# Kernel tuning notes

Hardware: AMD Instinct MI355X
Metric: run time of the kernel (lower is better)

## Reference

```python
import jax, jax.numpy as jnp
import numpy as np

INPUT_DIM = 2
COUNT_BINS = 16
BOUND = 5.0
FLOW_LENGTH = 4
HIDDEN = 256
MULT = 4 * COUNT_BINS - 1  # 63 param groups per dim (w:K, h:K, d:K-1, lam:K)
MIN_BIN = 1e-3
MIN_DERIV = 1e-3
MIN_LAMBDA = 0.025
N = 131072


def _masks():
    input_idx = np.arange(1, INPUT_DIM + 1)                  # [2]
    hidden_idx = np.arange(HIDDEN) % (INPUT_DIM - 1) + 1     # all ones for input_dim=2
    out_idx = np.tile(input_idx, MULT)                       # [126] -> [1,2,1,2,...]
    m1 = (hidden_idx[:, None] >= input_idx[None, :]).astype(np.float32)   # [H,2]
    m2 = (hidden_idx[:, None] >= hidden_idx[None, :]).astype(np.float32)  # [H,H]
    m3 = (out_idx[:, None] > hidden_idx[None, :]).astype(np.float32)      # [126,H]
    return jnp.asarray(m1), jnp.asarray(m2), jnp.asarray(m3)


def _made(z, W1, b1, W2, b2, W3, b3, m1, m2, m3):
    # masked MLP producing raw spline params, shape [..., MULT, input_dim]
    h = jax.nn.relu(z @ (W1 * m1).T + b1)
    h = jax.nn.relu(h @ (W2 * m2).T + b2)
    out = (h @ (W3 * m3).T + b3).reshape(z.shape[:-1] + (MULT, INPUT_DIM))
    K = COUNT_BINS
    sw = lambda t: jnp.swapaxes(t, -1, -2)  # -> [..., input_dim, K]
    w = sw(out[..., 0:K, :])
    hh = sw(out[..., K:2 * K, :])
    d = sw(out[..., 2 * K:3 * K - 1, :])
    lam = sw(out[..., 3 * K - 1:4 * K - 1, :])
    return w, hh, d, lam


def _spline(x, w_raw, h_raw, d_raw, l_raw):
    # Pyro monotonic linear rational spline (Dolatabadi et al.), forward only.
    K = COUNT_BINS
    left, right = -BOUND, BOUND
    w = jax.nn.softmax(w_raw, axis=-1)
    h = jax.nn.softmax(h_raw, axis=-1)
    d = jax.nn.softplus(d_raw)
    l = jax.nn.sigmoid(l_raw)

    widths = MIN_BIN + (1.0 - MIN_BIN * K) * w
    zpad = jnp.zeros(widths.shape[:-1] + (1,), widths.dtype)
    cw = jnp.concatenate([zpad, jnp.cumsum(widths, -1)], -1)
    cw = (right - left) * cw + left
    cw = cw.at[..., 0].set(left).at[..., -1].set(right)
    widths = cw[..., 1:] - cw[..., :-1]

    heights = MIN_BIN + (1.0 - MIN_BIN * K) * h
    ch = jnp.concatenate([zpad, jnp.cumsum(heights, -1)], -1)
    ch = (right - left) * ch + left
    ch = ch.at[..., 0].set(left).at[..., -1].set(right)
    heights = ch[..., 1:] - ch[..., :-1]

    deriv = MIN_DERIV + d
    onep = jnp.ones(deriv.shape[:-1] + (1,), deriv.dtype)
    deriv = jnp.concatenate([onep, deriv, onep], -1)  # boundary derivs = 1, [.., K+1]

    lam = MIN_LAMBDA + (1.0 - 2.0 * MIN_LAMBDA) * l

    inside = (x >= left) & (x <= right)
    xc = jnp.clip(x, left, right)

    bin_idx = jnp.clip(jnp.sum((xc[..., None] >= cw).astype(jnp.int32), -1) - 1, 0, K - 1)
    ib = bin_idx[..., None]
    g = lambda t: jnp.take_along_axis(t, ib, -1)[..., 0]
    x_k = g(cw)
    w_k = g(widths)
    y_k = g(ch)
    h_k = g(heights)
    d_k = g(deriv)
    d_k1 = jnp.take_along_axis(deriv, ib + 1, -1)[..., 0]
    lam_k = g(lam)

    wa = 1.0
    wb = jnp.sqrt(d_k / d_k1) * wa
    wc = (lam_k * wa * d_k + (1.0 - lam_k) * wb * d_k1) * (w_k / h_k)
    ya = y_k
    yb = h_k + y_k
    yc = ((1.0 - lam_k) * wa * ya + lam_k * wb * yb) / ((1.0 - lam_k) * wa + lam_k * wb)

    theta = (xc - x_k) / w_k
    left_seg = theta <= lam_k
    num = jnp.where(left_seg,
                    wa * ya * (lam_k - theta) + wc * yc * theta,
                    wc * yc * (1.0 - theta) + wb * yb * (theta - lam_k))
    den = jnp.where(left_seg,
                    wa * (lam_k - theta) + wc * theta,
                    wc * (1.0 - theta) + wb * (theta - lam_k))
    y = num / den
    return jnp.where(inside, y, x)  # identity outside [-B, B]


def setup_inputs() -> dict:
    key = jax.random.key(0)
    ks = jax.random.split(key, 7)
    s = 0.05
    return {
        "x": jax.random.normal(ks[0], (N, INPUT_DIM), jnp.float32),
        "W1": jax.random.normal(ks[1], (HIDDEN, INPUT_DIM), jnp.float32) * s,
        "b1": jax.random.normal(ks[2], (HIDDEN,), jnp.float32) * s,
        "W2": jax.random.normal(ks[3], (HIDDEN, HIDDEN), jnp.float32) * s,
        "b2": jax.random.normal(ks[4], (HIDDEN,), jnp.float32) * s,
        "W3": jax.random.normal(ks[5], (MULT * INPUT_DIM, HIDDEN), jnp.float32) * s,
        "b3": jax.random.normal(ks[6], (MULT * INPUT_DIM,), jnp.float32) * s,
    }


def reference(x, W1, b1, W2, b2, W3, b3):
    # forward(): apply the SAME shared spline transform flow_length times,
    # collecting intermediates zs (returned stacked: [L+1, N, 2]).
    m1, m2, m3 = _masks()
    z = x
    zs = [z]
    for _ in range(FLOW_LENGTH):
        w, hh, d, l = _made(z, W1, b1, W2, b2, W3, b3, m1, m2, m3)
        z = _spline(z, w, hh, d, l)
        zs.append(z)
    return jnp.stack(zs)
```

## Files before the change

kernel.cpp:

```cpp
#include <hip/hip_runtime.h>
#include <hip/hip_fp16.h>
#include <math.h>

#define N_SAMPLES 131072
#define HIDDEN    256
#define M_GRID    2048
#define REC       144
#define U_LO      (-8.0f)
#define DELTA     0.0078125f
#define INV_DELTA 128.0f
#define MT3       16

__device__ __attribute__((aligned(16))) float g_H2T[M_GRID * HIDDEN];
__device__ __attribute__((aligned(16))) float g_table[M_GRID * REC];
__device__ __attribute__((aligned(16))) float g_knots0[REC];

__device__ __forceinline__ float rcpf(float x) { return __builtin_amdgcn_rcpf(x); }

__device__ __forceinline__ float softplusf(float x) {
  return fmaxf(x, 0.0f) + log1pf(expf(-fabsf(x)));
}

__device__ __forceinline__ void unpack8(uint4 u, float* f) {
  float2 t;
  t = __half22float2(*(__half2*)&u.x); f[0] = t.x; f[1] = t.y;
  t = __half22float2(*(__half2*)&u.y); f[2] = t.x; f[3] = t.y;
  t = __half22float2(*(__half2*)&u.z); f[4] = t.x; f[5] = t.y;
  t = __half22float2(*(__half2*)&u.w); f[6] = t.x; f[7] = t.y;
}

__device__ void process_column(const float* __restrict__ raw, int stride,
                               float* __restrict__ rec) {
  float v[16];
  float cw[17], ch[17], dv[17], lm[16];
  float mx = -1e30f;
#pragma unroll
  for (int k = 0; k < 16; k++) { v[k] = raw[k * stride]; mx = fmaxf(mx, v[k]); }
  float s = 0.0f;
#pragma unroll
  for (int k = 0; k < 16; k++) { v[k] = expf(v[k] - mx); s += v[k]; }
  float scl = 0.984f / s;
  cw[0] = -5.0f;
  float a = 0.0f;
#pragma unroll
  for (int k = 0; k < 16; k++) {
    a += fmaf(v[k], scl, 0.001f);
    cw[k + 1] = fmaf(a, 10.0f, -5.0f);
  }
  cw[16] = 5.0f;
  mx = -1e30f;
#pragma unroll
  for (int k = 0; k < 16; k++) { v[k] = raw[(16 + k) * stride]; mx = fmaxf(mx, v[k]); }
  s = 0.0f;
#pragma unroll
  for (int k = 0; k < 16; k++) { v[k] = expf(v[k] - mx); s += v[k]; }
  scl = 0.984f / s;
  ch[0] = -5.0f;
  a = 0.0f;
#pragma unroll
  for (int k = 0; k < 16; k++) {
    a += fmaf(v[k], scl, 0.001f);
    ch[k + 1] = fmaf(a, 10.0f, -5.0f);
  }
  ch[16] = 5.0f;
  dv[0] = 1.0f; dv[16] = 1.0f;
#pragma unroll
  for (int j = 0; j < 15; j++) dv[j + 1] = 0.001f + softplusf(raw[(32 + j) * stride]);
#pragma unroll
  for (int k = 0; k < 16; k++) {
    float xx = raw[(47 + k) * stride];
    lm[k] = fmaf(0.95f, 1.0f / (1.0f + expf(-xx)), 0.025f);
  }
  unsigned int kn[8];
#pragma unroll
  for (int q = 0; q < 8; q++) {
    __half2 h2 = __floats2half2_rn(cw[2 * q], cw[2 * q + 1]);
    kn[q] = *(unsigned int*)&h2;
  }
  uint4* u4 = (uint4*)rec;
  u4[0] = make_uint4(kn[0], kn[1], kn[2], kn[3]);
  u4[1] = make_uint4(kn[4], kn[5], kn[6], kn[7]);
  float4* r4 = (float4*)rec;
  r4[2] = make_float4(0.0f, 0.0f, 0.0f, 0.0f);
  r4[3] = make_float4(0.0f, 0.0f, 0.0f, 0.0f);
#pragma unroll
  for (int k = 0; k < 16; k++) {
    r4[4 + 2 * k]     = make_float4(ch[k], ch[k + 1], dv[k], dv[k + 1]);
    r4[4 + 2 * k + 1] = make_float4(lm[k], cw[k], cw[k + 1], 0.0f);
  }
}

__device__ __forceinline__ float spline_eval(float z, float xk, float xk1,
                                             float yk, float yk1,
                                             float dk, float dk1, float lam) {
  float xc = fminf(fmaxf(z, -5.0f), 5.0f);
  float wk = xk1 - xk;
  float hk = yk1 - yk;
  float wb = __builtin_amdgcn_sqrtf(dk * rcpf(dk1));
  float wc = fmaf(lam, dk, (1.0f - lam) * wb * dk1) * wk * rcpf(hk);
  float ya = yk;
  float yb = yk + hk;
  float yc = fmaf(lam * wb, yb, (1.0f - lam) * ya) * rcpf(fmaf(lam, wb, 1.0f - lam));
  float th = (xc - xk) * rcpf(wk);
  bool left = th <= lam;
  float num = left ? fmaf(ya, lam - th, wc * yc * th)
                   : fmaf(wc * yc, 1.0f - th, wb * yb * (th - lam));
  float den = left ? fmaf(wc, th, lam - th)
                   : fmaf(wc, 1.0f - th, wb * (th - lam));
  float y = num * rcpf(den);
  bool inside = (z >= -5.0f) && (z <= 5.0f);
  return inside ? y : z;
}

__global__ __launch_bounds__(256) void k_gemm2(const float* __restrict__ W1,
                                               const float* __restrict__ b1,
                                               const float* __restrict__ W2,
                                               const float* __restrict__ b2) {
  __shared__ float sW[256 * 67];
  __shared__ float2 sAB[256];
  __shared__ float red[3 * 64 * 36];
  const int t = threadIdx.x;
  const int m0 = blockIdx.x * 32;
  const int o0 = blockIdx.y * 64;
  {
    const int ol = t >> 2, seg = t & 3;
    const float* src = W2 + (size_t)(o0 + ol) * 256 + 16 * seg;
#pragma unroll
    for (int c = 0; c < 4; c++) {
#pragma unroll
      for (int q = 0; q < 4; q++) {
        float4 v = *(const float4*)(src + 64 * c + 4 * q);
        const int k = 64 * c + 16 * seg + 4 * q;
        sW[(k + 0) * 67 + ol] = v.x;
        sW[(k + 1) * 67 + ol] = v.y;
        sW[(k + 2) * 67 + ol] = v.z;
        sW[(k + 3) * 67 + ol] = v.w;
      }
    }
  }
  sAB[t] = make_float2(W1[2 * t], b1[t]);
  __syncthreads();
  const int w = t >> 6, lane = t & 63;
  const int tp = lane >> 2, tm = lane & 3;
  const float u0 = fmaf((float)(m0 + 8 * tm), DELTA, U_LO);
  float acc[4][8] = {};
  const int kb = w * 64;
#pragma unroll 8
  for (int kk = 0; kk < 64; kk++) {
    const int k = kb + kk;
    float4 av = *(const float4*)&sW[k * 67 + 4 * tp];
    float2 ab = sAB[k];
    float t0 = fmaf(ab.x, u0, ab.y);
    float st = ab.x * DELTA;
    float h[8];
#pragma unroll
    for (int j = 0; j < 8; j++) h[j] = fmaxf(fmaf((float)j, st, t0), 0.0f);
#pragma unroll
    for (int i = 0; i < 4; i++) {
      const float aa = (i == 0) ? av.x : (i == 1) ? av.y : (i == 2) ? av.z : av.w;
#pragma unroll
      for (int j = 0; j < 8; j++) acc[i][j] = fmaf(aa, h[j], acc[i][j]);
    }
  }
  if (w > 0) {
#pragma unroll
    for (int i = 0; i < 4; i++) {
      *(float4*)&red[((w - 1) * 64 + lane) * 36 + 8 * i] =
          make_float4(acc[i][0], acc[i][1], acc[i][2], acc[i][3]);
      *(float4*)&red[((w - 1) * 64 + lane) * 36 + 8 * i + 4] =
          make_float4(acc[i][4], acc[i][5], acc[i][6], acc[i][7]);
    }
  }
  __syncthreads();
  if (w == 0) {
#pragma unroll
    for (int v = 0; v < 3; v++) {
#pragma unroll
      for (int i = 0; i < 4; i++) {
        float4 r0 = *(const float4*)&red[(v * 64 + lane) * 36 + 8 * i];
        float4 r1 = *(const float4*)&red[(v * 64 + lane) * 36 + 8 * i + 4];
        acc[i][0] += r0.x; acc[i][1] += r0.y; acc[i][2] += r0.z; acc[i][3] += r0.w;
        acc[i][4] += r1.x; acc[i][5] += r1.y; acc[i][6] += r1.z; acc[i][7] += r1.w;
      }
    }
    float4 bb = *(const float4*)&b2[o0 + 4 * tp];
#pragma unroll
    for (int j = 0; j < 8; j++) {
      float4 r;
      r.x = fmaxf(acc[0][j] + bb.x, 0.0f);
      r.y = fmaxf(acc[1][j] + bb.y, 0.0f);
      r.z = fmaxf(acc[2][j] + bb.z, 0.0f);
      r.w = fmaxf(acc[3][j] + bb.w, 0.0f);
      *(float4*)&g_H2T[(size_t)(m0 + 8 * tm + j) * 256 + o0 + 4 * tp] = r;
    }
  }
}

__global__ __launch_bounds__(256) void k_gemm3proc(const float* __restrict__ W3,
                                                   const float* __restrict__ b3) {
  __shared__ float sW[256 * 67];
  __shared__ float sH[256 * 20];
  __shared__ float raws[64 * 20];
  const int t = threadIdx.x;
  const int m0 = blockIdx.x * MT3;
  {
    const int ol = t >> 2, seg = t & 3;
    const int row = (ol < 63) ? (2 * ol + 1) : 1;
    const float* src = W3 + (size_t)row * 256 + 16 * seg;
#pragma unroll
    for (int c = 0; c < 4; c++) {
#pragma unroll
      for (int q = 0; q < 4; q++) {
        float4 v = *(const float4*)(src + 64 * c + 4 * q);
        const int k = 64 * c + 16 * seg + 4 * q;
        sW[(k + 0) * 67 + ol] = v.x;
        sW[(k + 1) * 67 + ol] = v.y;
        sW[(k + 2) * 67 + ol] = v.z;
        sW[(k + 3) * 67 + ol] = v.w;
      }
    }
  }
  {
    const int j = t & 15, c = t >> 4;
    const float* src = g_H2T + (size_t)(m0 + j) * 256 + 16 * c;
#pragma unroll
    for (int q = 0; q < 4; q++) {
      float4 v = *(const float4*)(src + 4 * q);
      const int k = 16 * c + 4 * q;
      sH[(k + 0) * 20 + j] = v.x;
      sH[(k + 1) * 20 + j] = v.y;
      sH[(k + 2) * 20 + j] = v.z;
      sH[(k + 3) * 20 + j] = v.w;
    }
  }
  __syncthreads();
  const int w = t >> 6, lane = t & 63;
  const int tp = lane >> 2, tm = lane & 3;
  float acc[4][4] = {};
  const int kb = w * 64;
#pragma unroll 8
  for (int kk = 0; kk < 64; kk++) {
    const int k = kb + kk;
    float4 av = *(const float4*)&sW[k * 67 + 4 * tp];
    float4 bv = *(const float4*)&sH[k * 20 + 4 * tm];
    acc[0][0] = fmaf(av.x, bv.x, acc[0][0]); acc[0][1] = fmaf(av.x, bv.y, acc[0][1]);
    acc[0][2] = fmaf(av.x, bv.z, acc[0][2]); acc[0][3] = fmaf(av.x, bv.w, acc[0][3]);
    acc[1][0] = fmaf(av.y, bv.x, acc[1][0]); acc[1][1] = fmaf(av.y, bv.y, acc[1][1]);
    acc[1][2] = fmaf(av.y, bv.z, acc[1][2]); acc[1][3] = fmaf(av.y, bv.w, acc[1][3]);
    acc[2][0] = fmaf(av.z, bv.x, acc[2][0]); acc[2][1] = fmaf(av.z, bv.y, acc[2][1]);
    acc[2][2] = fmaf(av.z, bv.z, acc[2][2]); acc[2][3] = fmaf(av.z, bv.w, acc[2][3]);
    acc[3][0] = fmaf(av.w, bv.x, acc[3][0]); acc[3][1] = fmaf(av.w, bv.y, acc[3][1]);
    acc[3][2] = fmaf(av.w, bv.z, acc[3][2]); acc[3][3] = fmaf(av.w, bv.w, acc[3][3]);
  }
  __syncthreads();
  if (w > 0) {
#pragma unroll
    for (int i = 0; i < 4; i++)
      *(float4*)&sH[((w - 1) * 64 + lane) * 20 + 4 * i] =
          make_float4(acc[i][0], acc[i][1], acc[i][2], acc[i][3]);
  }
  __syncthreads();
  if (w == 0) {
#pragma unroll
    for (int v = 0; v < 3; v++) {
#pragma unroll
      for (int i = 0; i < 4; i++) {
        float4 r = *(const float4*)&sH[(v * 64 + lane) * 20 + 4 * i];
        acc[i][0] += r.x; acc[i][1] += r.y; acc[i][2] += r.z; acc[i][3] += r.w;
      }
    }
#pragma unroll
    for (int i = 0; i < 4; i++) {
      const int p = 4 * tp + i;
      const int bi = (p < 63) ? (2 * p + 1) : 1;
      const float bias = b3[bi];
      *(float4*)&raws[p * 20 + 4 * tm] =
          make_float4(acc[i][0] + bias, acc[i][1] + bias,
                      acc[i][2] + bias, acc[i][3] + bias);
    }
  }
  __syncthreads();
  if (t < MT3) process_column(&raws[t], 20, g_table + (size_t)(m0 + t) * REC);
  if (t == 64 && blockIdx.x == 0) process_column(b3, 2, g_knots0);
}

__global__ __launch_bounds__(256) void k_main(const float* __restrict__ x,
                                              float* __restrict__ out) {
  __shared__ __attribute__((aligned(16))) float kn0[REC];
  for (int j = threadIdx.x; j < REC; j += 256) kn0[j] = g_knots0[j];
  __syncthreads();
  float kf0[16];
  {
    uint4 q0 = *(const uint4*)(kn0);
    uint4 q1 = *(const uint4*)(kn0 + 4);
    unpack8(q0, kf0);
    unpack8(q1, kf0 + 8);
  }
  const int i = blockIdx.x * 256 + threadIdx.x;
  const float2 xv = ((const float2*)x)[i];
  float z0 = xv.x, z1 = xv.y;
  ((float2*)out)[i] = xv;
  for (int t = 0; t < 4; t++) {
    float tt = (z0 - U_LO) * INV_DELTA;
    int i0 = (int)floorf(tt);
    i0 = min(max(i0, 0), M_GRID - 2);
    float f = fminf(fmaxf(tt - (float)i0, 0.0f), 1.0f);
    const float* r0 = g_table + (size_t)i0 * REC;
    float kf[16];
    {
      uint4 q0 = *(const uint4*)(r0);
      uint4 q1 = *(const uint4*)(r0 + 4);
      unpack8(q0, kf);
      unpack8(q1, kf + 8);
    }
    float xc1 = fminf(fmaxf(z1, -5.0f), 5.0f);
    int k1 = 0;
#pragma unroll
    for (int j = 1; j < 16; j++) k1 += (xc1 >= kf[j]) ? 1 : 0;
    const float* c0 = r0 + 16 + 8 * k1;
    float4 A0 = *(const float4*)c0;
    float4 A1 = *(const float4*)(c0 + 4);
    float4 B0 = *(const float4*)(c0 + REC);
    float4 B1 = *(const float4*)(c0 + REC + 4);
    float yk  = fmaf(f, B0.x - A0.x, A0.x);
    float yk1 = fmaf(f, B0.y - A0.y, A0.y);
    float dk  = fmaf(f, B0.z - A0.z, A0.z);
    float dk1 = fmaf(f, B0.w - A0.w, A0.w);
    float lam = fmaf(f, B1.x - A1.x, A1.x);
    float xk  = fmaf(f, B1.y - A1.y, A1.y);
    float xk1 = fmaf(f, B1.z - A1.z, A1.z);
    float z1n = spline_eval(z1, xk, xk1, yk, yk1, dk, dk1, lam);
    float xc0 = fminf(fmaxf(z0, -5.0f), 5.0f);
    int k0 = 0;
#pragma unroll
    for (int j = 1; j < 16; j++) k0 += (xc0 >= kf0[j]) ? 1 : 0;
    const float* c = kn0 + 16 + 8 * k0;
    float4 C0 = *(const float4*)c;
    float4 C1 = *(const float4*)(c + 4);
    float z0n = spline_eval(z0, C1.y, C1.z, C0.x, C0.y, C0.z, C0.w, C1.x);
    z0 = z0n; z1 = z1n;
    ((float2*)(out + (size_t)(t + 1) * (N_SAMPLES * 2)))[i] = make_float2(z0, z1);
  }
}

extern "C" void kernel_launch(void* const* d_in, const int* in_sizes, int n_in,
                              void* d_out, int out_size, void* d_ws, size_t ws_size,
                              hipStream_t stream) {
  const float* x  = (const float*)d_in[0];
  const float* W1 = (const float*)d_in[1];
  const float* b1 = (const float*)d_in[2];
  const float* W2 = (const float*)d_in[3];
  const float* b2 = (const float*)d_in[4];
  const float* W3 = (const float*)d_in[5];
  const float* b3 = (const float*)d_in[6];
  float* out = (float*)d_out;
  hipLaunchKernelGGL(k_gemm2, dim3(M_GRID / 32, 4), dim3(256), 0, stream, W1, b1, W2, b2);
  hipLaunchKernelGGL(k_gemm3proc, dim3(M_GRID / MT3), dim3(256), 0, stream, W3, b3);
  hipLaunchKernelGGL(k_main, dim3(N_SAMPLES / 256), dim3(256), 0, stream, x, out);
}
```

Baseline: 104.1 us.

## Store weights, hidden activations and spline table in packed fp16

Packs W2/W3 and the hidden activations into half2 in shared memory for both GEMM kernels, halving LDS footprint and read traffic per k-step. The spline lookup table records are also stored as half2, shrinking REC from 144 to 72 floats so the sampler's gathers fetch one uint4 per row instead of two float4s. This lowers shared-memory use and global table bandwidth, but adds conversion instructions and brings fp16 rounding error into the GEMM inputs and spline parameters, including knot positions and y-values.

Result: no change. 103.1 us (-1.0%).

```diff
diff --git a/kernel.cpp b/kernel.cpp
--- a/kernel.cpp
+++ b/kernel.cpp
@@ -5,11 +5,12 @@
 #define N_SAMPLES 131072
 #define HIDDEN    256
 #define M_GRID    2048
-#define REC       144
+#define REC       72
 #define U_LO      (-8.0f)
 #define DELTA     0.0078125f
 #define INV_DELTA 128.0f
 #define MT3       16
+#define STR2      69
 
 __device__ __attribute__((aligned(16))) float g_H2T[M_GRID * HIDDEN];
 __device__ __attribute__((aligned(16))) float g_table[M_GRID * REC];
@@ -19,6 +20,11 @@
 
 __device__ __forceinline__ float softplusf(float x) {
   return fmaxf(x, 0.0f) + log1pf(expf(-fabsf(x)));
+}
+
+__device__ __forceinline__ unsigned int packh2(float a, float b) {
+  __half2 h = __floats2half2_rn(a, b);
+  return *(unsigned int*)&h;
 }
 
 __device__ __forceinline__ void unpack8(uint4 u, float* f) {
@@ -71,22 +77,15 @@
     float xx = raw[(47 + k) * stride];
     lm[k] = fmaf(0.95f, 1.0f / (1.0f + expf(-xx)), 0.025f);
   }
-  unsigned int kn[8];
-#pragma unroll
-  for (int q = 0; q < 8; q++) {
-    __half2 h2 = __floats2half2_rn(cw[2 * q], cw[2 * q + 1]);
-    kn[q] = *(unsigned int*)&h2;
-  }
   uint4* u4 = (uint4*)rec;
-  u4[0] = make_uint4(kn[0], kn[1], kn[2], kn[3]);
-  u4[1] = make_uint4(kn[4], kn[5], kn[6], kn[7]);
-  float4* r4 = (float4*)rec;
-  r4[2] = make_float4(0.0f, 0.0f, 0.0f, 0.0f);
-  r4[3] = make_float4(0.0f, 0.0f, 0.0f, 0.0f);
+  u4[0] = make_uint4(packh2(cw[0], cw[1]),  packh2(cw[2], cw[3]),
+                     packh2(cw[4], cw[5]),  packh2(cw[6], cw[7]));
+  u4[1] = make_uint4(packh2(cw[8], cw[9]),  packh2(cw[10], cw[11]),
+                     packh2(cw[12], cw[13]), packh2(cw[14], cw[15]));
 #pragma unroll
   for (int k = 0; k < 16; k++) {
-    r4[4 + 2 * k]     = make_float4(ch[k], ch[k + 1], dv[k], dv[k + 1]);
-    r4[4 + 2 * k + 1] = make_float4(lm[k], cw[k], cw[k + 1], 0.0f);
+    u4[2 + k] = make_uint4(packh2(ch[k], ch[k + 1]), packh2(dv[k], dv[k + 1]),
+                           packh2(lm[k], cw[k]),     packh2(cw[k + 1], 0.0f));
   }
 }
 
@@ -116,7 +115,7 @@
                                                const float* __restrict__ b1,
                                                const float* __restrict__ W2,
                                                const float* __restrict__ b2) {
-  __shared__ float sW[256 * 67];
+  __shared__ unsigned int sW[128 * STR2];
   __shared__ float2 sAB[256];
   __shared__ float red[3 * 64 * 36];
   const int t = threadIdx.x;
@@ -130,11 +129,9 @@
 #pragma unroll
       for (int q = 0; q < 4; q++) {
         float4 v = *(const float4*)(src + 64 * c + 4 * q);
-        const int k = 64 * c + 16 * seg + 4 * q;
-        sW[(k + 0) * 67 + ol] = v.x;
-        sW[(k + 1) * 67 + ol] = v.y;
-        sW[(k + 2) * 67 + ol] = v.z;
-        sW[(k + 3) * 67 + ol] = v.w;
+        const int k2 = (64 * c + 16 * seg + 4 * q) >> 1;
+        sW[(k2 + 0) * STR2 + ol] = packh2(v.x, v.y);
+        sW[(k2 + 1) * STR2 + ol] = packh2(v.z, v.w);
       }
     }
   }
@@ -144,22 +141,35 @@
   const int tp = lane >> 2, tm = lane & 3;
   const float u0 = fmaf((float)(m0 + 8 * tm), DELTA, U_LO);
   float acc[4][8] = {};
-  const int kb = w * 64;
-#pragma unroll 8
-  for (int kk = 0; kk < 64; kk++) {
-    const int k = kb + kk;
-    float4 av = *(const float4*)&sW[k * 67 + 4 * tp];
-    float2 ab = sAB[k];
-    float t0 = fmaf(ab.x, u0, ab.y);
-    float st = ab.x * DELTA;
-    float h[8];
-#pragma unroll
-    for (int j = 0; j < 8; j++) h[j] = fmaxf(fmaf((float)j, st, t0), 0.0f);
-#pragma unroll
-    for (int i = 0; i < 4; i++) {
-      const float aa = (i == 0) ? av.x : (i == 1) ? av.y : (i == 2) ? av.z : av.w;
-#pragma unroll
-      for (int j = 0; j < 8; j++) acc[i][j] = fmaf(aa, h[j], acc[i][j]);
+  const int kb2 = w * 32;
+#pragma unroll 4
+  for (int kk = 0; kk < 32; kk++) {
+    const int k2 = kb2 + kk;
+    uint4 ap = *(const uint4*)&sW[k2 * STR2 + 4 * tp];
+    float2 a0 = __half22float2(*(__half2*)&ap.x);
+    float2 a1 = __half22float2(*(__half2*)&ap.y);
+    float2 a2 = __half22float2(*(__half2*)&ap.z);
+    float2 a3 = __half22float2(*(__half2*)&ap.w);
+    float2 abe = sAB[2 * k2];
+    float2 abo = sAB[2 * k2 + 1];
+    float t0e = fmaf(abe.x, u0, abe.y), ste = abe.x * DELTA;
+    float t0o = fmaf(abo.x, u0, abo.y), sto = abo.x * DELTA;
+    float he[8], ho[8];
+#pragma unroll
+    for (int j = 0; j < 8; j++) {
+      he[j] = fmaxf(fmaf((float)j, ste, t0e), 0.0f);
+      ho[j] = fmaxf(fmaf((float)j, sto, t0o), 0.0f);
+    }
+#pragma unroll
+    for (int j = 0; j < 8; j++) {
+      acc[0][j] = fmaf(a0.x, he[j], acc[0][j]);
+      acc[1][j] = fmaf(a1.x, he[j], acc[1][j]);
+      acc[2][j] = fmaf(a2.x, he[j], acc[2][j]);
+      acc[3][j] = fmaf(a3.x, he[j], acc[3][j]);
+      acc[0][j] = fmaf(a0.y, ho[j], acc[0][j]);
+      acc[1][j] = fmaf(a1.y, ho[j], acc[1][j]);
+      acc[2][j] = fmaf(a2.y, ho[j], acc[2][j]);
+      acc[3][j] = fmaf(a3.y, ho[j], acc[3][j]);
     }
   }
   if (w > 0) {
@@ -198,8 +208,9 @@
 
 __global__ __launch_bounds__(256) void k_gemm3proc(const float* __restrict__ W3,
                                                    const float* __restrict__ b3) {
-  __shared__ float sW[256 * 67];
-  __shared__ float sH[256 * 20];
+  __shared__ unsigned int sW[128 * STR2];
+  __shared__ unsigned int sH[128 * 17];
+  __shared__ float red[3 * 64 * 20];
   __shared__ float raws[64 * 20];
   const int t = threadIdx.x;
   const int m0 = blockIdx.x * MT3;
@@ -212,11 +223,9 @@
 #pragma unroll
       for (int q = 0; q < 4; q++) {
         float4 v = *(const float4*)(src + 64 * c + 4 * q);
-        const int k = 64 * c + 16 * seg + 4 * q;
-        sW[(k + 0) * 67 + ol] = v.x;
-        sW[(k + 1) * 67 + ol] = v.y;
-        sW[(k + 2) * 67 + ol] = v.z;
-        sW[(k + 3) * 67 + ol] = v.w;
+        const int k2 = (64 * c + 16 * seg + 4 * q) >> 1;
+        sW[(k2 + 0) * STR2 + ol] = packh2(v.x, v.y);
+        sW[(k2 + 1) * STR2 + ol] = packh2(v.z, v.w);
       }
     }
   }
@@ -226,37 +235,46 @@
 #pragma unroll
     for (int q = 0; q < 4; q++) {
       float4 v = *(const float4*)(src + 4 * q);
-      const int k = 16 * c + 4 * q;
-      sH[(k + 0) * 20 + j] = v.x;
-      sH[(k + 1) * 20 + j] = v.y;
-      sH[(k + 2) * 20 + j] = v.z;
-      sH[(k + 3) * 20 + j] = v.w;
+      const int k2 = (16 * c + 4 * q) >> 1;
+      sH[(k2 + 0) * 17 + j] = packh2(v.x, v.y);
+      sH[(k2 + 1) * 17 + j] = packh2(v.z, v.w);
     }
   }
   __syncthreads();
   const int w = t >> 6, lane = t & 63;
   const int tp = lane >> 2, tm = lane & 3;
   float acc[4][4] = {};
-  const int kb = w * 64;
-#pragma unroll 8
-  for (int kk = 0; kk < 64; kk++) {
-    const int k = kb + kk;
-    float4 av = *(const float4*)&sW[k * 67 + 4 * tp];
-    float4 bv = *(const float4*)&sH[k * 20 + 4 * tm];
-    acc[0][0] = fmaf(av.x, bv.x, acc[0][0]); acc[0][1] = fmaf(av.x, bv.y, acc[0][1]);
-    acc[0][2] = fmaf(av.x, bv.z, acc[0][2]); acc[0][3] = fmaf(av.x, bv.w, acc[0][3]);
-    acc[1][0] = fmaf(av.y, bv.x, acc[1][0]); acc[1][1] = fmaf(av.y, bv.y, acc[1][1]);
-    acc[1][2] = fmaf(av.y, bv.z, acc[1][2]); acc[1][3] = fmaf(av.y, bv.w, acc[1][3]);
-    acc[2][0] = fmaf(av.z, bv.x, acc[2][0]); acc[2][1] = fmaf(av.z, bv.y, acc[2][1]);
-    acc[2][2] = fmaf(av.z, bv.z, acc[2][2]); acc[2][3] = fmaf(av.z, bv.w, acc[2][3]);
-    acc[3][0] = fmaf(av.w, bv.x, acc[3][0]); acc[3][1] = fmaf(av.w, bv.y, acc[3][1]);
-    acc[3][2] = fmaf(av.w, bv.z, acc[3][2]); acc[3][3] = fmaf(av.w, bv.w, acc[3][3]);
-  }
-  __syncthreads();
+  const int kb2 = w * 32;
+#pragma unroll 4
+  for (int kk = 0; kk < 32; kk++) {
+    const int k2 = kb2 + kk;
+    uint4 ap = *(const uint4*)&sW[k2 * STR2 + 4 * tp];
+    uint4 bp = *(const uint4*)&sH[k2 * 17 + 4 * tm];
+    float2 a0 = __half22float2(*(__half2*)&ap.x);
+    float2 a1 = __half22float2(*(__half2*)&ap.y);
+    float2 a2 = __half22float2(*(__half2*)&ap.z);
+    float2 a3 = __half22float2(*(__half2*)&ap.w);
+    float2 b0 = __half22float2(*(__half2*)&bp.x);
+    float2 b1v = __half22float2(*(__half2*)&bp.y);
+    float2 b2v = __half22float2(*(__half2*)&bp.z);
+    float2 b3v = __half22float2(*(__half2*)&bp.w);
+    float ae[4] = {a0.x, a1.x, a2.x, a3.x};
+    float ao[4] = {a0.y, a1.y, a2.y, a3.y};
+    float be[4] = {b0.x, b1v.x, b2v.x, b3v.x};
+    float bo[4] = {b0.y, b1v.y, b2v.y, b3v.y};
+#pragma unroll
+    for (int i = 0; i < 4; i++) {
+#pragma unroll
+      for (int j = 0; j < 4; j++) {
+        acc[i][j] = fmaf(ae[i], be[j], acc[i][j]);
+        acc[i][j] = fmaf(ao[i], bo[j], acc[i][j]);
+      }
+    }
+  }
   if (w > 0) {
 #pragma unroll
     for (int i = 0; i < 4; i++)
-      *(float4*)&sH[((w - 1) * 64 + lane) * 20 + 4 * i] =
+      *(float4*)&red[((w - 1) * 64 + lane) * 20 + 4 * i] =
           make_float4(acc[i][0], acc[i][1], acc[i][2], acc[i][3]);
   }
   __syncthreads();
@@ -265,7 +283,7 @@
     for (int v = 0; v < 3; v++) {
 #pragma unroll
       for (int i = 0; i < 4; i++) {
-        float4 r = *(const float4*)&sH[(v * 64 + lane) * 20 + 4 * i];
+        float4 r = *(const float4*)&red[(v * 64 + lane) * 20 + 4 * i];
         acc[i][0] += r.x; acc[i][1] += r.y; acc[i][2] += r.z; acc[i][3] += r.w;
       }
     }
@@ -317,27 +335,35 @@
     int k1 = 0;
 #pragma unroll
     for (int j = 1; j < 16; j++) k1 += (xc1 >= kf[j]) ? 1 : 0;
-    const float* c0 = r0 + 16 + 8 * k1;
-    float4 A0 = *(const float4*)c0;
-    float4 A1 = *(const float4*)(c0 + 4);
-    float4 B0 = *(const float4*)(c0 + REC);
-    float4 B1 = *(const float4*)(c0 + REC + 4);
-    float yk  = fmaf(f, B0.x - A0.x, A0.x);
-    float yk1 = fmaf(f, B0.y - A0.y, A0.y);
-    float dk  = fmaf(f, B0.z - A0.z, A0.z);
-    float dk1 = fmaf(f, B0.w - A0.w, A0.w);
-    float lam = fmaf(f, B1.x - A1.x, A1.x);
-    float xk  = fmaf(f, B1.y - A1.y, A1.y);
-    float xk1 = fmaf(f, B1.z - A1.z, A1.z);
+    const float* c0 = r0 + 8 + 4 * k1;
+    uint4 A = *(const uint4*)c0;
+    uint4 B = *(const uint4*)(c0 + REC);
+    float2 Ay = __half22float2(*(__half2*)&A.x);
+    float2 Ad = __half22float2(*(__half2*)&A.y);
+    float2 Al = __half22float2(*(__half2*)&A.z);
+    float2 Ax = __half22float2(*(__half2*)&A.w);
+    float2 By = __half22float2(*(__half2*)&B.x);
+    float2 Bd = __half22float2(*(__half2*)&B.y);
+    float2 Bl = __half22float2(*(__half2*)&B.z);
+    float2 Bx = __half22float2(*(__half2*)&B.w);
+    float yk  = fmaf(f, By.x - Ay.x, Ay.x);
+    float yk1 = fmaf(f, By.y - Ay.y, Ay.y);
+    float dk  = fmaf(f, Bd.x - Ad.x, Ad.x);
+    float dk1 = fmaf(f, Bd.y - Ad.y, Ad.y);
+    float lam = fmaf(f, Bl.x - Al.x, Al.x);
+    float xk  = fmaf(f, Bl.y - Al.y, Al.y);
+    float xk1 = fmaf(f, Bx.x - Ax.x, Ax.x);
     float z1n = spline_eval(z1, xk, xk1, yk, yk1, dk, dk1, lam);
     float xc0 = fminf(fmaxf(z0, -5.0f), 5.0f);
     int k0 = 0;
 #pragma unroll
     for (int j = 1; j < 16; j++) k0 += (xc0 >= kf0[j]) ? 1 : 0;
-    const float* c = kn0 + 16 + 8 * k0;
-    float4 C0 = *(const float4*)c;
-    float4 C1 = *(const float4*)(c + 4);
-    float z0n = spline_eval(z0, C1.y, C1.z, C0.x, C0.y, C0.z, C0.w, C1.x);
+    uint4 C = *(const uint4*)&kn0[8 + 4 * k0];
+    float2 Cy = __half22float2(*(__half2*)&C.x);
+    float2 Cd = __half22float2(*(__half2*)&C.y);
+    float2 Cl = __half22float2(*(__half2*)&C.z);
+    float2 Cx = __half22float2(*(__half2*)&C.w);
+    float z0n = spline_eval(z0, Cl.y, Cx.x, Cy.x, Cy.y, Cd.x, Cd.y, Cl.x);
     z0 = z0n; z1 = z1n;
     ((float2*)(out + (size_t)(t + 1) * (N_SAMPLES * 2)))[i] = make_float2(z0, z1);
   }
```
